# Kernel tuning notes

Measured on AMD Instinct MI355X. Metric: run time of the kernel, lower is better.

The kernel has to match this reference:

```python
import jax, jax.numpy as jnp
import numpy as np

N = 100000
E = 1600000
D = 128

def setup_inputs() -> dict:
    key = jax.random.key(0)
    ks = jax.random.split(key, 8)
    s = 1.0 / np.sqrt(D)
    x = jax.random.normal(ks[0], (N, D), dtype=jnp.float32)
    Wl1 = jax.random.uniform(ks[1], (D, D), jnp.float32, -s, s)
    bl1 = jnp.zeros((D,), jnp.float32)
    Wr1 = jax.random.uniform(ks[2], (D, D), jnp.float32, -s, s)
    Wl2 = jax.random.uniform(ks[3], (D, D), jnp.float32, -s, s)
    bl2 = jnp.zeros((D,), jnp.float32)
    Wr2 = jax.random.uniform(ks[4], (D, D), jnp.float32, -s, s)
    edge_index = jax.random.randint(ks[5], (2, E), 0, N, dtype=jnp.int64)
    return {"x": x, "Wl1": Wl1, "bl1": bl1, "Wr1": Wr1,
            "Wl2": Wl2, "bl2": bl2, "Wr2": Wr2, "edge_index": edge_index}

def _sage_layer(x, src, dst, Wl, bl, Wr, num_nodes):
    # mean aggregation of source features onto destination nodes
    msg = x[src]                                               # [E, D] gather
    ssum = jax.ops.segment_sum(msg, dst, num_segments=num_nodes)
    deg = jax.ops.segment_sum(jnp.ones((src.shape[0], 1), x.dtype), dst,
                              num_segments=num_nodes)
    agg = ssum / jnp.maximum(deg, 1.0)
    # out = lin_l(agg) + lin_r(x); lin_l has bias, lin_r has none (PyG SAGEConv)
    return agg @ Wl + bl + x @ Wr

def reference(x, Wl1, bl1, Wr1, Wl2, bl2, Wr2, edge_index):
    src, dst = edge_index[0], edge_index[1]
    n = x.shape[0]
    h = jax.nn.relu(_sage_layer(x, src, dst, Wl1, bl1, Wr1, n))
    # dropout is identity at inference
    h = jax.nn.relu(_sage_layer(h, src, dst, Wl2, bl2, Wr2, n))
    return h
```

## Files before the change

kernel.cpp:

```cpp
#include <hip/hip_runtime.h>
#include <cstdint>

typedef float f4 __attribute__((ext_vector_type(4)));
typedef float f2 __attribute__((ext_vector_type(2)));
typedef short bfv8 __attribute__((ext_vector_type(8)));

__device__ inline f4 f4_zero(){ f4 v = {0.f,0.f,0.f,0.f}; return v; }

__device__ inline uint32_t f2bf(float f){
    uint32_t u = __float_as_uint(f);
    return (u + 0x7fffu + ((u >> 16) & 1u)) >> 16;
}
__device__ inline uint32_t pack_bf2(float a, float b){
    return f2bf(a) | (f2bf(b) << 16);
}
__device__ inline f2 bf2_unpack(uint32_t v){
    f2 r;
    r[0] = __uint_as_float(v << 16);
    r[1] = __uint_as_float(v & 0xffff0000u);
    return r;
}

#define PB 256

__global__ __launch_bounds__(256) void k_tobf16(const f4* __restrict__ in,
                                                uint2* __restrict__ out, int n4){
    int i = blockIdx.x * 256 + threadIdx.x;
    if (i >= n4) return;
    f4 v = in[i];
    uint2 o;
    o.x = pack_bf2(v[0], v[1]);
    o.y = pack_bf2(v[2], v[3]);
    out[i] = o;
}

__global__ void k_detect(const uint32_t* __restrict__ p, int* __restrict__ flag){
    __shared__ int nz;
    if (threadIdx.x == 0) nz = 0;
    __syncthreads();
    int local = 0;
    for (int i = threadIdx.x; i < 2048; i += blockDim.x)
        if (p[2*i + 1] != 0u) local = 1;
    if (local) atomicOr(&nz, 1);
    __syncthreads();
    if (threadIdx.x == 0) *flag = (nz == 0) ? 1 : 0;
}

__global__ __launch_bounds__(1024) void k_hist(const void* __restrict__ eidx, int E, int NB,
                                               const int* __restrict__ flag,
                                               int* __restrict__ blkhist){
    __shared__ int lh[1024];
    int t = threadIdx.x, blk = blockIdx.x;
    for (int i = t; i < NB; i += 1024) lh[i] = 0;
    __syncthreads();
    int R = (E + PB - 1) / PB;
    int s = blk * R, e_end = s + R < E ? s + R : E;
    bool is64 = (*flag != 0);
    const uint32_t* p32 = (const uint32_t*)eidx;
    const int*      pi  = (const int*)eidx;
    for (int e = s + t; e < e_end; e += 1024){
        int d = is64 ? (int)p32[2*(size_t)(E + e)] : pi[(size_t)E + e];
        atomicAdd(&lh[d >> 7], 1);
    }
    __syncthreads();
    for (int i = t; i < NB; i += 1024)
        blkhist[(size_t)i * PB + blk] = lh[i];
}

__global__ __launch_bounds__(PB) void k_btot(const int* __restrict__ blkhist,
                                             int* __restrict__ tot){
    int b = blockIdx.x, t = threadIdx.x, lane = t & 63, w = t >> 6;
    int v = blkhist[(size_t)b * PB + t];
    #pragma unroll
    for (int off = 32; off; off >>= 1) v += __shfl_down(v, off, 64);
    __shared__ int ws[4];
    if (lane == 0) ws[w] = v;
    __syncthreads();
    if (t == 0) tot[b] = ws[0] + ws[1] + ws[2] + ws[3];
}

__global__ __launch_bounds__(1024) void k_bscan(const int* __restrict__ tot, int n,
                                                int* __restrict__ coff){
    int t = threadIdx.x, lane = t & 63, w = t >> 6;
    int v = (t < n) ? tot[t] : 0;
    int x = v;
    #pragma unroll
    for (int off = 1; off < 64; off <<= 1){
        int u = __shfl_up(x, off, 64);
        if (lane >= off) x += u;
    }
    __shared__ int ws[16];
    if (lane == 63) ws[w] = x;
    __syncthreads();
    if (w == 0 && lane < 16){
        int y = ws[lane];
        #pragma unroll
        for (int off = 1; off < 16; off <<= 1){
            int u = __shfl_up(y, off, 64);
            if (lane >= off) y += u;
        }
        ws[lane] = y;
    }
    __syncthreads();
    int incl = x + (w ? ws[w - 1] : 0);
    if (t < n)     coff[t] = incl - v;
    if (t == n - 1) coff[n] = incl;
}

__global__ __launch_bounds__(PB) void k_boff(const int* __restrict__ blkhist,
                                             const int* __restrict__ coff,
                                             int* __restrict__ offs){
    int b = blockIdx.x, t = threadIdx.x, lane = t & 63, w = t >> 6;
    int h = blkhist[(size_t)b * PB + t];
    int x = h;
    #pragma unroll
    for (int off = 1; off < 64; off <<= 1){
        int u = __shfl_up(x, off, 64);
        if (lane >= off) x += u;
    }
    __shared__ int ws[4];
    if (lane == 63) ws[w] = x;
    __syncthreads();
    int add = 0;
    for (int j = 0; j < w; ++j) add += ws[j];
    offs[(size_t)b * PB + t] = coff[b] + add + x - h;
}

__global__ __launch_bounds__(1024) void k_scatter(const void* __restrict__ eidx, int E, int NB,
                                                  const int* __restrict__ flag,
                                                  const int* __restrict__ offs,
                                                  uint32_t* __restrict__ bucketed){
    __shared__ int cur[1024];
    int t = threadIdx.x, blk = blockIdx.x;
    for (int i = t; i < NB; i += 1024) cur[i] = offs[(size_t)i * PB + blk];
    __syncthreads();
    int R = (E + PB - 1) / PB;
    int s = blk * R, e_end = s + R < E ? s + R : E;
    bool is64 = (*flag != 0);
    const uint32_t* p32 = (const uint32_t*)eidx;
    const int*      pi  = (const int*)eidx;
    for (int e = s + t; e < e_end; e += 1024){
        int sv, dv;
        if (is64){ sv = (int)p32[2*(size_t)e]; dv = (int)p32[2*(size_t)(E + e)]; }
        else     { sv = pi[e];                 dv = pi[(size_t)E + e]; }
        int b = dv >> 7;
        int pos = atomicAdd(&cur[b], 1);
        bucketed[pos] = ((uint32_t)(dv & 127) << 17) | (uint32_t)sv;
    }
}

__global__ __launch_bounds__(1024) void k_bucketsort(const uint32_t* __restrict__ bucketed,
                                                     const int* __restrict__ coff,
                                                     int* __restrict__ esrc,
                                                     int* __restrict__ rowptr,
                                                     int N, int E, int NB){
    __shared__ int hist[128], cur[128], wtot[2];
    int b = blockIdx.x, t = threadIdx.x;
    if (t < 128) hist[t] = 0;
    __syncthreads();
    int s = coff[b], e_end = coff[b + 1];
    for (int i = s + t; i < e_end; i += 1024)
        atomicAdd(&hist[bucketed[i] >> 17], 1);
    __syncthreads();
    int x = 0, v = 0;
    if (t < 128){
        int lane = t & 63;
        v = hist[t]; x = v;
        #pragma unroll
        for (int off = 1; off < 64; off <<= 1){
            int u = __shfl_up(x, off, 64);
            if (lane >= off) x += u;
        }
        if (lane == 63) wtot[t >> 6] = x;
    }
    __syncthreads();
    if (t < 128){
        int w = t >> 6;
        int excl = x - v + (w ? wtot[0] : 0);
        int abs0 = s + excl;
        cur[t] = abs0;
        int node = b * 128 + t;
        if (node < N) rowptr[node] = abs0;
    }
    if (b == NB - 1 && t == 0) rowptr[N] = E;
    __syncthreads();
    for (int i = s + t; i < e_end; i += 1024){
        uint32_t val = bucketed[i];
        int r = (int)(val >> 17);
        int pos = atomicAdd(&cur[r], 1);
        esrc[pos] = (int)(val & 0x1FFFFu);
    }
}

__global__ __launch_bounds__(256) void k_aggregate(const uint32_t* __restrict__ featb,
                                                   const int* __restrict__ rowptr,
                                                   const int* __restrict__ esrc,
                                                   uint32_t* __restrict__ aggb, int N){
    int node = blockIdx.x * 4 + (threadIdx.x >> 6);
    if (node >= N) return;
    int lane = threadIdx.x & 63;
    int b = rowptr[node], e = rowptr[node + 1];
    f2 a0 = {0.f,0.f}, a1 = {0.f,0.f}, a2 = {0.f,0.f}, a3 = {0.f,0.f};
    f2 a4 = {0.f,0.f}, a5 = {0.f,0.f}, a6 = {0.f,0.f}, a7 = {0.f,0.f};
    for (int base = b; base < e; base += 64){
        int m = e - base; if (m > 64) m = 64;
        int idx = (lane < m) ? esrc[base + lane] : 0;
        int j = 0;
        for (; j + 8 <= m; j += 8){
            int s0 = __shfl(idx, j,     64);
            int s1 = __shfl(idx, j + 1, 64);
            int s2 = __shfl(idx, j + 2, 64);
            int s3 = __shfl(idx, j + 3, 64);
            int s4 = __shfl(idx, j + 4, 64);
            int s5 = __shfl(idx, j + 5, 64);
            int s6 = __shfl(idx, j + 6, 64);
            int s7 = __shfl(idx, j + 7, 64);
            uint32_t g0 = featb[(size_t)s0 * 64 + lane];
            uint32_t g1 = featb[(size_t)s1 * 64 + lane];
            uint32_t g2 = featb[(size_t)s2 * 64 + lane];
            uint32_t g3 = featb[(size_t)s3 * 64 + lane];
            uint32_t g4 = featb[(size_t)s4 * 64 + lane];
            uint32_t g5 = featb[(size_t)s5 * 64 + lane];
            uint32_t g6 = featb[(size_t)s6 * 64 + lane];
            uint32_t g7 = featb[(size_t)s7 * 64 + lane];
            a0 += bf2_unpack(g0); a1 += bf2_unpack(g1);
            a2 += bf2_unpack(g2); a3 += bf2_unpack(g3);
            a4 += bf2_unpack(g4); a5 += bf2_unpack(g5);
            a6 += bf2_unpack(g6); a7 += bf2_unpack(g7);
        }
        for (; j < m; ++j){
            int s0 = __shfl(idx, j, 64);
            a0 += bf2_unpack(featb[(size_t)s0 * 64 + lane]);
        }
    }
    f2 acc = ((a0 + a1) + (a2 + a3)) + ((a4 + a5) + (a6 + a7));
    int deg = e - b;
    float scl = 1.0f / (float)(deg > 1 ? deg : 1);
    aggb[(size_t)node * 64 + lane] = pack_bf2(acc[0] * scl, acc[1] * scl);
}

__global__ __launch_bounds__(256) void k_wprep(const float* __restrict__ Wl,
                                               const float* __restrict__ Wr,
                                               uint32_t* __restrict__ Bsw){
    int t = blockIdx.x * 256 + threadIdx.x;
    int s = t >> 9, ct = (t >> 6) & 7, l = t & 63;
    int k0 = s * 32 + (l >> 4) * 8;
    int c  = ct * 16 + (l & 15);
    unsigned short e[8];
    #pragma unroll
    for (int j = 0; j < 8; ++j){
        int k = k0 + j;
        float v = (k < 128) ? Wl[(size_t)k * 128 + c] : Wr[(size_t)(k - 128) * 128 + c];
        e[j] = (unsigned short)f2bf(v);
    }
    uint32_t* o = Bsw + (size_t)t * 4;
    o[0] = (uint32_t)e[0] | ((uint32_t)e[1] << 16);
    o[1] = (uint32_t)e[2] | ((uint32_t)e[3] << 16);
    o[2] = (uint32_t)e[4] | ((uint32_t)e[5] << 16);
    o[3] = (uint32_t)e[6] | ((uint32_t)e[7] << 16);
}

__global__ __launch_bounds__(256) void k_sage_mfma(
    const uint32_t* __restrict__ A1b, const uint32_t* __restrict__ A2b,
    const uint32_t* __restrict__ Bsw, const float* __restrict__ bias,
    float* __restrict__ outf, uint32_t* __restrict__ outbf, int M)
{
    int tid = threadIdx.x;
    int w = tid >> 6, l = tid & 63;
    int l15 = l & 15, l4 = l >> 4;
    int row = blockIdx.x * 64 + w * 16 + l15;
    int rowc = row < M ? row : M - 1;
    const char* a1p = (const char*)(A1b + (size_t)rowc * 64) + l4 * 16;
    const char* a2p = (const char*)(A2b + (size_t)rowc * 64) + l4 * 16;
    const char* bp  = (const char*)Bsw + (size_t)l * 16;

    f4 acc[8];
    #pragma unroll
    for (int ct = 0; ct < 8; ++ct) acc[ct] = f4_zero();

    #pragma unroll
    for (int s = 0; s < 8; ++s){
        bfv8 a = *(const bfv8*)((s < 4 ? a1p : a2p) + (s & 3) * 64);
        #pragma unroll
        for (int ct = 0; ct < 8; ++ct){
            bfv8 b = *(const bfv8*)(bp + (size_t)(s * 8 + ct) * 1024);
            acc[ct] = __builtin_amdgcn_mfma_f32_16x16x32_bf16(a, b, acc[ct], 0, 0, 0);
        }
    }

    int orow0 = blockIdx.x * 64 + w * 16 + l4 * 4;
    #pragma unroll
    for (int ct = 0; ct < 8; ++ct){
        int col = ct * 16 + l15;
        float bb = bias[col];
        #pragma unroll
        for (int r = 0; r < 4; ++r){
            int orow = orow0 + r;
            if (orow < M){
                float v = acc[ct][r] + bb;
                v = v > 0.f ? v : 0.f;
                if (outf)  outf[(size_t)orow * 128 + col] = v;
                if (outbf) ((unsigned short*)outbf)[(size_t)orow * 128 + col] =
                               (unsigned short)f2bf(v);
            }
        }
    }
}

extern "C" void kernel_launch(void* const* d_in, const int* in_sizes, int n_in,
                              void* d_out, int out_size, void* d_ws, size_t ws_size,
                              hipStream_t stream) {
    const float* x    = (const float*)d_in[0];
    const float* Wl1  = (const float*)d_in[1];
    const float* bl1  = (const float*)d_in[2];
    const float* Wr1  = (const float*)d_in[3];
    const float* Wl2  = (const float*)d_in[4];
    const float* bl2  = (const float*)d_in[5];
    const float* Wr2  = (const float*)d_in[6];
    const void*  eidx = d_in[7];
    float* out = (float*)d_out;

    const int N  = in_sizes[0] / 128;
    const int E  = in_sizes[7] / 2;
    const int NB = (N + 127) >> 7;

    char* ws = (char*)d_ws;
    size_t off = 0;
    auto alloc = [&](size_t bytes) -> void* {
        void* p = ws + off;
        off += (bytes + 255) & ~(size_t)255;
        return p;
    };
    int*      flag     = (int*)     alloc(4);
    int*      blkhist  = (int*)     alloc((size_t)NB * PB * 4);
    int*      tot      = (int*)     alloc((size_t)NB * 4);
    int*      coff     = (int*)     alloc((size_t)(NB + 1) * 4);
    int*      offs     = (int*)     alloc((size_t)NB * PB * 4);
    int*      esrc     = (int*)     alloc((size_t)E * 4);
    int*      rowptr   = (int*)     alloc((size_t)(N + 1) * 4);
    uint32_t* bsw1     = (uint32_t*)alloc(65536);
    uint32_t* bsw2     = (uint32_t*)alloc(65536);
    size_t uA = (size_t)E * 4 > (size_t)N * 256 ? (size_t)E * 4 : (size_t)N * 256;
    uint32_t* unionA   = (uint32_t*)alloc(uA);
    uint32_t* bucketed = unionA;
    uint32_t* aggb     = unionA;
    uint32_t* unionB   = (uint32_t*)alloc((size_t)N * 256);
    uint32_t* xbf      = unionB;
    uint32_t* hbf      = unionB;

    const int GB = (N + 63) / 64;

    k_tobf16    <<<(N * 32 + 255) / 256, 256, 0, stream>>>((const f4*)x, (uint2*)xbf, N * 32);
    k_wprep     <<<16, 256, 0, stream>>>(Wl1, Wr1, bsw1);
    k_wprep     <<<16, 256, 0, stream>>>(Wl2, Wr2, bsw2);
    k_detect    <<<1, 256, 0, stream>>>((const uint32_t*)eidx, flag);
    k_hist      <<<PB, 1024, 0, stream>>>(eidx, E, NB, flag, blkhist);
    k_btot      <<<NB, PB,   0, stream>>>(blkhist, tot);
    k_bscan     <<<1, 1024,  0, stream>>>(tot, NB, coff);
    k_boff      <<<NB, PB,   0, stream>>>(blkhist, coff, offs);
    k_scatter   <<<PB, 1024, 0, stream>>>(eidx, E, NB, flag, offs, bucketed);
    k_bucketsort<<<NB, 1024, 0, stream>>>(bucketed, coff, esrc, rowptr, N, E, NB);

    k_aggregate<<<(N + 3) / 4, 256, 0, stream>>>(xbf, rowptr, esrc, aggb, N);
    k_sage_mfma<<<GB, 256, 0, stream>>>(aggb, xbf, bsw1, bl1, nullptr, hbf, N);

    k_aggregate<<<(N + 3) / 4, 256, 0, stream>>>(hbf, rowptr, esrc, aggb, N);
    k_sage_mfma<<<GB, 256, 0, stream>>>(aggb, hbf, bsw2, bl2, out, nullptr, N);
}
```

Measured before the change: 356.1 us.

## Fuse offset-scan kernels into one and widen aggregate gathers to 8-byte loads

Drops the partition block count from 256 to 64 and replaces the three offset kernels (block totals, scan, per-block offsets) with one single-block kernel that sums and scans histogram rows with int4 loads, cutting two launches. The aggregate kernel now has each half-wave handle a different edge with 8-byte loads per lane, then combines the halves with a cross-half shuffle. The aim is fewer launches and fewer, wider gather instructions, at the cost of fewer histogram/scatter blocks (less parallelism there) and serial per-thread row work in the single-block scan.

```diff
diff --git a/kernel.cpp b/kernel.cpp
--- a/kernel.cpp
+++ b/kernel.cpp
@@ -21,7 +21,7 @@
     return r;
 }
 
-#define PB 256
+#define PB 64
 
 __global__ __launch_bounds__(256) void k_tobf16(const f4* __restrict__ in,
                                                 uint2* __restrict__ out, int n4){
@@ -67,29 +67,32 @@
         blkhist[(size_t)i * PB + blk] = lh[i];
 }
 
-__global__ __launch_bounds__(PB) void k_btot(const int* __restrict__ blkhist,
-                                             int* __restrict__ tot){
-    int b = blockIdx.x, t = threadIdx.x, lane = t & 63, w = t >> 6;
-    int v = blkhist[(size_t)b * PB + t];
-    #pragma unroll
-    for (int off = 32; off; off >>= 1) v += __shfl_down(v, off, 64);
-    __shared__ int ws[4];
-    if (lane == 0) ws[w] = v;
-    __syncthreads();
-    if (t == 0) tot[b] = ws[0] + ws[1] + ws[2] + ws[3];
-}
-
-__global__ __launch_bounds__(1024) void k_bscan(const int* __restrict__ tot, int n,
-                                                int* __restrict__ coff){
+__global__ __launch_bounds__(1024) void k_offsets(const int* __restrict__ blkhist,
+                                                  int NB,
+                                                  int* __restrict__ coff,
+                                                  int* __restrict__ offs){
+    __shared__ int tot_s[1024];
+    __shared__ int excl_s[1024];
+    __shared__ int ws[16];
     int t = threadIdx.x, lane = t & 63, w = t >> 6;
-    int v = (t < n) ? tot[t] : 0;
-    int x = v;
+    int v = 0;
+    if (t < NB){
+        const int4* row = (const int4*)(blkhist + (size_t)t * PB);
+        #pragma unroll
+        for (int i = 0; i < PB/4; ++i){
+            int4 q = row[i];
+            v += q.x + q.y + q.z + q.w;
+        }
+    }
+    tot_s[t] = v;
+    __syncthreads();
+    int x = tot_s[t];
+    int vv = x;
     #pragma unroll
     for (int off = 1; off < 64; off <<= 1){
         int u = __shfl_up(x, off, 64);
         if (lane >= off) x += u;
     }
-    __shared__ int ws[16];
     if (lane == 63) ws[w] = x;
     __syncthreads();
     if (w == 0 && lane < 16){
@@ -103,27 +106,26 @@
     }
     __syncthreads();
     int incl = x + (w ? ws[w - 1] : 0);
-    if (t < n)     coff[t] = incl - v;
-    if (t == n - 1) coff[n] = incl;
-}
-
-__global__ __launch_bounds__(PB) void k_boff(const int* __restrict__ blkhist,
-                                             const int* __restrict__ coff,
-                                             int* __restrict__ offs){
-    int b = blockIdx.x, t = threadIdx.x, lane = t & 63, w = t >> 6;
-    int h = blkhist[(size_t)b * PB + t];
-    int x = h;
-    #pragma unroll
-    for (int off = 1; off < 64; off <<= 1){
-        int u = __shfl_up(x, off, 64);
-        if (lane >= off) x += u;
-    }
-    __shared__ int ws[4];
-    if (lane == 63) ws[w] = x;
-    __syncthreads();
-    int add = 0;
-    for (int j = 0; j < w; ++j) add += ws[j];
-    offs[(size_t)b * PB + t] = coff[b] + add + x - h;
+    int excl = incl - vv;
+    excl_s[t] = excl;
+    if (t < NB)      coff[t] = excl;
+    if (t == NB - 1) coff[NB] = incl;
+    __syncthreads();
+    if (t < NB){
+        const int4* row  = (const int4*)(blkhist + (size_t)t * PB);
+        int4*       orow = (int4*)(offs + (size_t)t * PB);
+        int run = excl_s[t];
+        #pragma unroll
+        for (int i = 0; i < PB/4; ++i){
+            int4 q = row[i];
+            int4 o;
+            o.x = run; run += q.x;
+            o.y = run; run += q.y;
+            o.z = run; run += q.z;
+            o.w = run; run += q.w;
+            orow[i] = o;
+        }
+    }
 }
 
 __global__ __launch_bounds__(1024) void k_scatter(const void* __restrict__ eidx, int E, int NB,
@@ -199,44 +201,50 @@
     int node = blockIdx.x * 4 + (threadIdx.x >> 6);
     if (node >= N) return;
     int lane = threadIdx.x & 63;
+    int half = lane >> 5;
+    int l8   = lane & 31;
     int b = rowptr[node], e = rowptr[node + 1];
-    f2 a0 = {0.f,0.f}, a1 = {0.f,0.f}, a2 = {0.f,0.f}, a3 = {0.f,0.f};
-    f2 a4 = {0.f,0.f}, a5 = {0.f,0.f}, a6 = {0.f,0.f}, a7 = {0.f,0.f};
+    f2 c0lo={0.f,0.f}, c0hi={0.f,0.f}, c1lo={0.f,0.f}, c1hi={0.f,0.f};
+    f2 c2lo={0.f,0.f}, c2hi={0.f,0.f}, c3lo={0.f,0.f}, c3hi={0.f,0.f};
     for (int base = b; base < e; base += 64){
         int m = e - base; if (m > 64) m = 64;
         int idx = (lane < m) ? esrc[base + lane] : 0;
         int j = 0;
         for (; j + 8 <= m; j += 8){
-            int s0 = __shfl(idx, j,     64);
-            int s1 = __shfl(idx, j + 1, 64);
-            int s2 = __shfl(idx, j + 2, 64);
-            int s3 = __shfl(idx, j + 3, 64);
-            int s4 = __shfl(idx, j + 4, 64);
-            int s5 = __shfl(idx, j + 5, 64);
-            int s6 = __shfl(idx, j + 6, 64);
-            int s7 = __shfl(idx, j + 7, 64);
-            uint32_t g0 = featb[(size_t)s0 * 64 + lane];
-            uint32_t g1 = featb[(size_t)s1 * 64 + lane];
-            uint32_t g2 = featb[(size_t)s2 * 64 + lane];
-            uint32_t g3 = featb[(size_t)s3 * 64 + lane];
-            uint32_t g4 = featb[(size_t)s4 * 64 + lane];
-            uint32_t g5 = featb[(size_t)s5 * 64 + lane];
-            uint32_t g6 = featb[(size_t)s6 * 64 + lane];
-            uint32_t g7 = featb[(size_t)s7 * 64 + lane];
-            a0 += bf2_unpack(g0); a1 += bf2_unpack(g1);
-            a2 += bf2_unpack(g2); a3 += bf2_unpack(g3);
-            a4 += bf2_unpack(g4); a5 += bf2_unpack(g5);
-            a6 += bf2_unpack(g6); a7 += bf2_unpack(g7);
-        }
-        for (; j < m; ++j){
-            int s0 = __shfl(idx, j, 64);
-            a0 += bf2_unpack(featb[(size_t)s0 * 64 + lane]);
-        }
-    }
-    f2 acc = ((a0 + a1) + (a2 + a3)) + ((a4 + a5) + (a6 + a7));
-    int deg = e - b;
-    float scl = 1.0f / (float)(deg > 1 ? deg : 1);
-    aggb[(size_t)node * 64 + lane] = pack_bf2(acc[0] * scl, acc[1] * scl);
+            int s0 = __shfl(idx, j     + half, 64);
+            int s1 = __shfl(idx, j + 2 + half, 64);
+            int s2 = __shfl(idx, j + 4 + half, 64);
+            int s3 = __shfl(idx, j + 6 + half, 64);
+            uint2 g0 = *(const uint2*)(featb + (size_t)s0 * 64 + l8 * 2);
+            uint2 g1 = *(const uint2*)(featb + (size_t)s1 * 64 + l8 * 2);
+            uint2 g2 = *(const uint2*)(featb + (size_t)s2 * 64 + l8 * 2);
+            uint2 g3 = *(const uint2*)(featb + (size_t)s3 * 64 + l8 * 2);
+            c0lo += bf2_unpack(g0.x); c0hi += bf2_unpack(g0.y);
+            c1lo += bf2_unpack(g1.x); c1hi += bf2_unpack(g1.y);
+            c2lo += bf2_unpack(g2.x); c2hi += bf2_unpack(g2.y);
+            c3lo += bf2_unpack(g3.x); c3hi += bf2_unpack(g3.y);
+        }
+        for (; j < m; j += 2){
+            int jj = j + half;
+            int s0 = __shfl(idx, jj < m ? jj : j, 64);
+            uint2 g = *(const uint2*)(featb + (size_t)s0 * 64 + l8 * 2);
+            if (jj < m){ c0lo += bf2_unpack(g.x); c0hi += bf2_unpack(g.y); }
+        }
+    }
+    f2 lo = (c0lo + c1lo) + (c2lo + c3lo);
+    f2 hi = (c0hi + c1hi) + (c2hi + c3hi);
+    lo[0] += __shfl_xor(lo[0], 32, 64);
+    lo[1] += __shfl_xor(lo[1], 32, 64);
+    hi[0] += __shfl_xor(hi[0], 32, 64);
+    hi[1] += __shfl_xor(hi[1], 32, 64);
+    if (half == 0){
+        int deg = e - b;
+        float scl = 1.0f / (float)(deg > 1 ? deg : 1);
+        uint2 o;
+        o.x = pack_bf2(lo[0] * scl, lo[1] * scl);
+        o.y = pack_bf2(hi[0] * scl, hi[1] * scl);
+        *(uint2*)(aggb + (size_t)node * 64 + l8 * 2) = o;
+    }
 }
 
 __global__ __launch_bounds__(256) void k_wprep(const float* __restrict__ Wl,
@@ -333,7 +341,6 @@
     };
     int*      flag     = (int*)     alloc(4);
     int*      blkhist  = (int*)     alloc((size_t)NB * PB * 4);
-    int*      tot      = (int*)     alloc((size_t)NB * 4);
     int*      coff     = (int*)     alloc((size_t)(NB + 1) * 4);
     int*      offs     = (int*)     alloc((size_t)NB * PB * 4);
     int*      esrc     = (int*)     alloc((size_t)E * 4);
@@ -355,9 +362,7 @@
     k_wprep     <<<16, 256, 0, stream>>>(Wl2, Wr2, bsw2);
     k_detect    <<<1, 256, 0, stream>>>((const uint32_t*)eidx, flag);
     k_hist      <<<PB, 1024, 0, stream>>>(eidx, E, NB, flag, blkhist);
-    k_btot      <<<NB, PB,   0, stream>>>(blkhist, tot);
-    k_bscan     <<<1, 1024,  0, stream>>>(tot, NB, coff);
-    k_boff      <<<NB, PB,   0, stream>>>(blkhist, coff, offs);
+    k_offsets   <<<1, 1024, 0, stream>>>(blkhist, NB, coff, offs);
     k_scatter   <<<PB, 1024, 0, stream>>>(eidx, E, NB, flag, offs, bucketed);
     k_bucketsort<<<NB, 1024, 0, stream>>>(bucketed, coff, esrc, rowptr, N, E, NB);
 
```

Measured after the change: 393.8 us. 1.11x slower.
